# Kernel optimization log

Hardware: AMD Instinct MI355X
Metric: run time of the kernel (lower is better)

## Reference

```python
import jax, jax.numpy as jnp
import numpy as np

N, E = 50000, 1600000
FEAT, HID, HEADS = 256, 64, 2
NEG_SLOPE = 0.2


def gat_conv(x, src, dst, W, att_src, att_dst, bias, heads, out_ch):
    """PyG GATConv (concat=True, self-loops already appended to src/dst)."""
    n = x.shape[0]
    h = (x @ W).reshape(n, heads, out_ch)                      # [N,H,C]
    a_src = jnp.einsum('nhc,hc->nh', h, att_src)               # [N,H]
    a_dst = jnp.einsum('nhc,hc->nh', h, att_dst)               # [N,H]
    alpha = jax.nn.leaky_relu(a_src[src] + a_dst[dst], NEG_SLOPE)  # [E',H]
    # segment softmax over incoming edges of each dst node
    amax = jax.ops.segment_max(alpha, dst, num_segments=n)
    alpha = jnp.exp(alpha - amax[dst])
    denom = jax.ops.segment_sum(alpha, dst, num_segments=n)
    alpha = alpha / (denom[dst] + 1e-16)
    msg = h[src] * alpha[..., None]                            # [E',H,C]
    out = jax.ops.segment_sum(msg, dst, num_segments=n)        # [N,H,C]
    return out.reshape(n, heads * out_ch) + bias


def setup_inputs() -> dict:
    key = jax.random.key(0)
    ks = jax.random.split(key, 10)
    x = jax.random.normal(ks[0], (N, FEAT), dtype=jnp.float32)
    edge_index = jax.random.randint(ks[1], (2, E), 0, N, dtype=jnp.int64)
    s1 = 1.0 / np.sqrt(FEAT)
    s2 = 1.0 / np.sqrt(HID * HEADS)
    sa = 1.0 / np.sqrt(HID)
    return {
        'x': x,
        'edge_index': edge_index,
        'W1': jax.random.uniform(ks[2], (FEAT, HEADS * HID), jnp.float32, -s1, s1),
        'att_src1': jax.random.uniform(ks[3], (HEADS, HID), jnp.float32, -sa, sa),
        'att_dst1': jax.random.uniform(ks[4], (HEADS, HID), jnp.float32, -sa, sa),
        'b1': jnp.zeros((HEADS * HID,), jnp.float32),
        'W2': jax.random.uniform(ks[5], (HEADS * HID, HID), jnp.float32, -s2, s2),
        'att_src2': jax.random.uniform(ks[6], (1, HID), jnp.float32, -sa, sa),
        'att_dst2': jax.random.uniform(ks[7], (1, HID), jnp.float32, -sa, sa),
        'b2': jnp.zeros((HID,), jnp.float32),
    }


def reference(x, edge_index, W1, att_src1, att_dst1, b1, W2, att_src2, att_dst2, b2):
    n = x.shape[0]
    loop = jnp.arange(n, dtype=edge_index.dtype)
    src = jnp.concatenate([edge_index[0], loop])   # add self loops (PyG default)
    dst = jnp.concatenate([edge_index[1], loop])
    h = gat_conv(x, src, dst, W1, att_src1, att_dst1, b1, HEADS, HID)
    h = jax.nn.relu(h)  # dropout is identity in eval mode
    h = gat_conv(h, src, dst, W2, att_src2, att_dst2, b2, 1, HID)
    return jax.nn.log_softmax(h, axis=1)
```

## Files before the change

kernel.cpp:

```cpp
#include <hip/hip_runtime.h>
#include <hip/hip_bf16.h>
#include <math.h>

typedef short bf16x8 __attribute__((ext_vector_type(8)));
typedef float f32x4 __attribute__((ext_vector_type(4)));

#define BSHIFT 7
#define BWIDTH 128
#define PCHUNK 4096

__global__ void prep_kernel(int* __restrict__ bcnt,
                            const float* __restrict__ W1, const float* __restrict__ W2,
                            __hip_bfloat16* __restrict__ W1t,
                            __hip_bfloat16* __restrict__ W2t) {
    if (blockIdx.x == 0) {
        bcnt[threadIdx.x] = 0;
        bcnt[threadIdx.x + 256] = 0;
        return;
    }
    int idx = (blockIdx.x - 1) * 256 + threadIdx.x;
    const int n1 = 128 * 256;
    if (idx < n1) {
        int nn = idx >> 8, kk = idx & 255;
        W1t[idx] = __float2bfloat16(W1[kk * 128 + nn]);
    } else {
        int j = idx - n1;
        if (j < 64 * 128) {
            int nn = j >> 7, kk = j & 127;
            W2t[j] = __float2bfloat16(W2[kk * 64 + nn]);
        }
    }
}

__global__ __launch_bounds__(256) void bucket_hist(const int* __restrict__ ei, int E,
                                                   int* __restrict__ bcnt) {
    __shared__ int h[512];
    int tid = threadIdx.x;
    for (int i = tid; i < 512; i += 256) h[i] = 0;
    __syncthreads();
    int start = blockIdx.x * PCHUNK;
    int cnt = min(PCHUNK, E - start);
    for (int i = tid; i < cnt; i += 256)
        atomicAdd(&h[ei[E + start + i] >> BSHIFT], 1);
    __syncthreads();
    for (int i = tid; i < 512; i += 256)
        if (h[i]) atomicAdd(&bcnt[i], h[i]);
}

__global__ __launch_bounds__(512) void bucket_scan(const int* __restrict__ bcnt,
                                                   int* __restrict__ bbase,
                                                   int* __restrict__ bcur,
                                                   int nbk, int n) {
    __shared__ int s[512];
    int tid = threadIdx.x;
    int nodes = 0;
    if (tid < nbk) nodes = min(BWIDTH, n - (tid << BSHIFT));
    int v = (tid < nbk) ? bcnt[tid] + nodes : 0;
    s[tid] = v;
    __syncthreads();
    #pragma unroll
    for (int o = 1; o < 512; o <<= 1) {
        int t = (tid >= o) ? s[tid - o] : 0;
        __syncthreads();
        s[tid] += t;
        __syncthreads();
    }
    if (tid < nbk) {
        int ex = s[tid] - v;
        bbase[tid] = ex;
        bcur[tid] = ex - (tid << BSHIFT);
    }
    if (tid == nbk) bbase[nbk] = s[tid];
}

__global__ __launch_bounds__(256) void partition_edges(const int* __restrict__ ei, int E,
                                                       int* __restrict__ bcur,
                                                       int* __restrict__ tmp) {
    __shared__ int2 stage[PCHUNK];
    __shared__ int h[512];
    __shared__ int lbase[512];
    int tid = threadIdx.x;
    int start = blockIdx.x * PCHUNK;
    int cnt = min(PCHUNK, E - start);
    for (int i = tid; i < 512; i += 256) h[i] = 0;
    __syncthreads();
    for (int i = tid; i < cnt; i += 256) {
        int s = ei[start + i];
        int d = ei[E + start + i];
        stage[i] = make_int2(s, d);
        atomicAdd(&h[d >> BSHIFT], 1);
    }
    __syncthreads();
    for (int i = tid; i < 512; i += 256) {
        if (h[i] > 0) lbase[i] = atomicAdd(&bcur[i], h[i]);
        h[i] = 0;
    }
    __syncthreads();
    for (int i = tid; i < cnt; i += 256) {
        int2 e = stage[i];
        int b = e.y >> BSHIFT;
        int r = atomicAdd(&h[b], 1);
        tmp[lbase[b] + r] = (e.x << BSHIFT) | (e.y & (BWIDTH - 1));
    }
}

__global__ __launch_bounds__(256) void bucket_csr(const int* __restrict__ bbase,
                                                  const int* __restrict__ tmp,
                                                  int* __restrict__ offs,
                                                  int* __restrict__ srcs,
                                                  int n, int nbk) {
    __shared__ int cnt[BWIDTH];
    __shared__ int sa[BWIDTH];
    __shared__ int cur[BWIDTH];
    int b = blockIdx.x;
    int tid = threadIdx.x;
    int node0 = b << BSHIFT;
    int nnodes = min(BWIDTH, n - node0);
    int cb = bbase[b];
    int ce = bbase[b + 1];
    int tb = cb - node0;
    int ecnt = (ce - cb) - nnodes;

    if (tid < BWIDTH) cnt[tid] = (tid < nnodes) ? 1 : 0;
    __syncthreads();
    for (int i = tid; i < ecnt; i += 256)
        atomicAdd(&cnt[tmp[tb + i] & (BWIDTH - 1)], 1);
    __syncthreads();
    if (tid < BWIDTH) sa[tid] = cnt[tid];
    __syncthreads();
    #pragma unroll
    for (int o = 1; o < BWIDTH; o <<= 1) {
        int v = 0;
        if (tid < BWIDTH) { v = sa[tid]; if (tid >= o) v += sa[tid - o]; }
        __syncthreads();
        if (tid < BWIDTH) sa[tid] = v;
        __syncthreads();
    }
    if (tid < BWIDTH) {
        int ex = sa[tid] - cnt[tid];
        if (tid < nnodes) {
            offs[node0 + tid] = cb + ex;
            srcs[cb + ex] = node0 + tid;
        }
        cur[tid] = ex + (tid < nnodes ? 1 : 0);
    }
    if (b == nbk - 1 && tid == 0) offs[n] = ce;
    __syncthreads();
    for (int i = tid; i < ecnt; i += 256) {
        int e = tmp[tb + i];
        int li = e & (BWIDTH - 1);
        int r = atomicAdd(&cur[li], 1);
        srcs[cb + r] = e >> BSHIFT;
    }
}

template <bool A_BF16, int NT, int HEADS>
__global__ __launch_bounds__(256) void gemm_att(
    const void* __restrict__ Av, const __hip_bfloat16* __restrict__ Bt,
    __hip_bfloat16* __restrict__ C,
    const float* __restrict__ atts, const float* __restrict__ attd,
    float* __restrict__ a_s, float* __restrict__ a_d, int M, int K) {
    constexpr int N = NT * 16;
    __shared__ __hip_bfloat16 As[64][40];
    int tid = threadIdx.x;
    int w = tid >> 6, l = tid & 63;
    int q = l >> 4, m16 = l & 15;
    int bm = blockIdx.x * 64;

    int lr = tid >> 2, lseg = tid & 3;
    int arow = bm + lr; if (arow >= M) arow = M - 1;

    f32x4 acc[NT];
    #pragma unroll
    for (int t = 0; t < NT; t++) acc[t] = (f32x4){0.f, 0.f, 0.f, 0.f};

    for (int kc = 0; kc < K; kc += 32) {
        if (A_BF16) {
            const __hip_bfloat16* A = (const __hip_bfloat16*)Av;
            uint4 v = *(const uint4*)(A + (size_t)arow * K + kc + lseg * 8);
            *(uint4*)&As[lr][lseg * 8] = v;
        } else {
            const float* A = (const float*)Av;
            float4 v0 = *(const float4*)(A + (size_t)arow * K + kc + lseg * 8);
            float4 v1 = *(const float4*)(A + (size_t)arow * K + kc + lseg * 8 + 4);
            union { __hip_bfloat16 h[8]; uint4 u; } tmp;
            tmp.h[0] = __float2bfloat16(v0.x); tmp.h[1] = __float2bfloat16(v0.y);
            tmp.h[2] = __float2bfloat16(v0.z); tmp.h[3] = __float2bfloat16(v0.w);
            tmp.h[4] = __float2bfloat16(v1.x); tmp.h[5] = __float2bfloat16(v1.y);
            tmp.h[6] = __float2bfloat16(v1.z); tmp.h[7] = __float2bfloat16(v1.w);
            *(uint4*)&As[lr][lseg * 8] = tmp.u;
        }
        __syncthreads();
        bf16x8 a = *(const bf16x8*)&As[w * 16 + m16][q * 8];
        #pragma unroll
        for (int t = 0; t < NT; t++) {
            bf16x8 b = *(const bf16x8*)(Bt + (size_t)(t * 16 + m16) * K + kc + q * 8);
            acc[t] = __builtin_amdgcn_mfma_f32_16x16x32_bf16(a, b, acc[t], 0, 0, 0);
        }
        __syncthreads();
    }

    #pragma unroll
    for (int t = 0; t < NT; t++) {
        #pragma unroll
        for (int r = 0; r < 4; r++) {
            int row = bm + w * 16 + q * 4 + r;
            if (row < M) C[(size_t)row * N + t * 16 + m16] = __float2bfloat16(acc[t][r]);
        }
    }

    float ps[HEADS][4], pd[HEADS][4];
    #pragma unroll
    for (int hh = 0; hh < HEADS; hh++)
        #pragma unroll
        for (int r = 0; r < 4; r++) { ps[hh][r] = 0.f; pd[hh][r] = 0.f; }
    #pragma unroll
    for (int t = 0; t < NT; t++) {
        int ch = t * 16 + m16;
        float asw = atts[ch], adw = attd[ch];
        int hh = (HEADS == 2) ? (t >> 2) : 0;
        #pragma unroll
        for (int r = 0; r < 4; r++) {
            ps[hh][r] = fmaf(acc[t][r], asw, ps[hh][r]);
            pd[hh][r] = fmaf(acc[t][r], adw, pd[hh][r]);
        }
    }
    #pragma unroll
    for (int o = 1; o < 16; o <<= 1) {
        #pragma unroll
        for (int hh = 0; hh < HEADS; hh++)
            #pragma unroll
            for (int r = 0; r < 4; r++) {
                ps[hh][r] += __shfl_xor(ps[hh][r], o);
                pd[hh][r] += __shfl_xor(pd[hh][r], o);
            }
    }
    if (m16 == 0) {
        #pragma unroll
        for (int r = 0; r < 4; r++) {
            int row = bm + w * 16 + q * 4 + r;
            if (row < M) {
                if (HEADS == 2) {
                    a_s[row * 2]     = ps[0][r];
                    a_s[row * 2 + 1] = ps[1][r];
                    a_d[row * 2]     = pd[0][r];
                    a_d[row * 2 + 1] = pd[1][r];
                } else {
                    a_s[row] = ps[0][r];
                    a_d[row] = pd[0][r];
                }
            }
        }
    }
}

__device__ __forceinline__ float leaky(float r) {
    return r < 0.f ? 0.2f * r : r;
}

__device__ __forceinline__ void unpack2(unsigned u, float& lo, float& hi) {
    lo = __uint_as_float(u << 16);
    hi = __uint_as_float(u & 0xffff0000u);
}

__global__ __launch_bounds__(256) void edge_agg_l1(
    const int* __restrict__ offs, const int* __restrict__ srcs,
    const __hip_bfloat16* __restrict__ h1, const float* __restrict__ asv,
    const float* __restrict__ adv, const float* __restrict__ bias,
    __hip_bfloat16* __restrict__ out, int n) {
    int d = (blockIdx.x * blockDim.x + threadIdx.x) >> 6;
    int lane = threadIdx.x & 63;
    if (d >= n) return;
    int start = offs[d], end = offs[d + 1];
    float ad0 = adv[2 * d], ad1 = adv[2 * d + 1];

    int sub = lane & 15;
    int g = lane >> 4;
    int ch0 = sub * 8;
    int hsel = sub >> 3;

    float s0 = 0.f, s1 = 0.f;
    float acc[8];
    #pragma unroll
    for (int k = 0; k < 8; k++) acc[k] = 0.f;

    for (int base = start; base < end; base += 64) {
        int cnt = min(64, end - base);
        int s_l = 0;
        float e0 = 0.f, e1 = 0.f;
        if (lane < cnt) {
            s_l = srcs[base + lane];
            float2 a = *(const float2*)(asv + 2 * s_l);
            e0 = __expf(leaky(a.x + ad0));
            e1 = __expf(leaky(a.y + ad1));
        }
        s0 += e0;
        s1 += e1;

        int steps = (cnt + 3) >> 2;
        int jj = 0;
        for (; jj + 2 <= steps; jj += 2) {
            int eA = jj * 4 + g, eB = eA + 4;
            float w0A = __shfl(e0, eA), w1A = __shfl(e1, eA);
            int sA = __shfl(s_l, eA);
            float w0B = __shfl(e0, eB), w1B = __shfl(e1, eB);
            int sB = __shfl(s_l, eB);
            float wA = hsel ? w1A : w0A;
            float wB = hsel ? w1B : w0B;
            uint4 vA = *(const uint4*)(h1 + (size_t)sA * 128 + ch0);
            uint4 vB = *(const uint4*)(h1 + (size_t)sB * 128 + ch0);
            float f0, f1, f2, f3, f4, f5, f6, f7;
            unpack2(vA.x, f0, f1); unpack2(vA.y, f2, f3);
            unpack2(vA.z, f4, f5); unpack2(vA.w, f6, f7);
            acc[0] = fmaf(wA, f0, acc[0]); acc[1] = fmaf(wA, f1, acc[1]);
            acc[2] = fmaf(wA, f2, acc[2]); acc[3] = fmaf(wA, f3, acc[3]);
            acc[4] = fmaf(wA, f4, acc[4]); acc[5] = fmaf(wA, f5, acc[5]);
            acc[6] = fmaf(wA, f6, acc[6]); acc[7] = fmaf(wA, f7, acc[7]);
            unpack2(vB.x, f0, f1); unpack2(vB.y, f2, f3);
            unpack2(vB.z, f4, f5); unpack2(vB.w, f6, f7);
            acc[0] = fmaf(wB, f0, acc[0]); acc[1] = fmaf(wB, f1, acc[1]);
            acc[2] = fmaf(wB, f2, acc[2]); acc[3] = fmaf(wB, f3, acc[3]);
            acc[4] = fmaf(wB, f4, acc[4]); acc[5] = fmaf(wB, f5, acc[5]);
            acc[6] = fmaf(wB, f6, acc[6]); acc[7] = fmaf(wB, f7, acc[7]);
        }
        if (jj < steps) {
            int eA = jj * 4 + g;
            float w0A = __shfl(e0, eA), w1A = __shfl(e1, eA);
            int sA = __shfl(s_l, eA);
            float wA = hsel ? w1A : w0A;
            uint4 vA = *(const uint4*)(h1 + (size_t)sA * 128 + ch0);
            float f0, f1, f2, f3, f4, f5, f6, f7;
            unpack2(vA.x, f0, f1); unpack2(vA.y, f2, f3);
            unpack2(vA.z, f4, f5); unpack2(vA.w, f6, f7);
            acc[0] = fmaf(wA, f0, acc[0]); acc[1] = fmaf(wA, f1, acc[1]);
            acc[2] = fmaf(wA, f2, acc[2]); acc[3] = fmaf(wA, f3, acc[3]);
            acc[4] = fmaf(wA, f4, acc[4]); acc[5] = fmaf(wA, f5, acc[5]);
            acc[6] = fmaf(wA, f6, acc[6]); acc[7] = fmaf(wA, f7, acc[7]);
        }
    }
    #pragma unroll
    for (int o = 16; o < 64; o <<= 1)
        #pragma unroll
        for (int k = 0; k < 8; k++) acc[k] += __shfl_xor(acc[k], o);
    #pragma unroll
    for (int o = 1; o < 64; o <<= 1) {
        s0 += __shfl_xor(s0, o);
        s1 += __shfl_xor(s1, o);
    }

    if (lane < 16) {
        float invh = 1.f / ((hsel ? s1 : s0) + 1e-16f);
        float4 b0 = *(const float4*)(bias + ch0);
        float4 b1 = *(const float4*)(bias + ch0 + 4);
        union { __hip_bfloat16 h[8]; uint4 u; } o2;
        o2.h[0] = __float2bfloat16(fmaxf(fmaf(acc[0], invh, b0.x), 0.f));
        o2.h[1] = __float2bfloat16(fmaxf(fmaf(acc[1], invh, b0.y), 0.f));
        o2.h[2] = __float2bfloat16(fmaxf(fmaf(acc[2], invh, b0.z), 0.f));
        o2.h[3] = __float2bfloat16(fmaxf(fmaf(acc[3], invh, b0.w), 0.f));
        o2.h[4] = __float2bfloat16(fmaxf(fmaf(acc[4], invh, b1.x), 0.f));
        o2.h[5] = __float2bfloat16(fmaxf(fmaf(acc[5], invh, b1.y), 0.f));
        o2.h[6] = __float2bfloat16(fmaxf(fmaf(acc[6], invh, b1.z), 0.f));
        o2.h[7] = __float2bfloat16(fmaxf(fmaf(acc[7], invh, b1.w), 0.f));
        *(uint4*)(out + (size_t)d * 128 + ch0) = o2.u;
    }
}

__global__ __launch_bounds__(256) void edge_agg_l2(
    const int* __restrict__ offs, const int* __restrict__ srcs,
    const __hip_bfloat16* __restrict__ h2, const float* __restrict__ asv,
    const float* __restrict__ adv, const float* __restrict__ bias,
    float* __restrict__ out, int n) {
    int d = (blockIdx.x * blockDim.x + threadIdx.x) >> 6;
    int lane = threadIdx.x & 63;
    if (d >= n) return;
    int start = offs[d], end = offs[d + 1];
    float ad = adv[d];

    int sub = lane & 7;
    int g = lane >> 3;
    int ch0 = sub * 8;

    float ssum = 0.f;
    float acc[8];
    #pragma unroll
    for (int k = 0; k < 8; k++) acc[k] = 0.f;

    for (int base = start; base < end; base += 64) {
        int cnt = min(64, end - base);
        int s_l = 0;
        float ew = 0.f;
        if (lane < cnt) {
            s_l = srcs[base + lane];
            ew = __expf(leaky(asv[s_l] + ad));
        }
        ssum += ew;

        int steps = (cnt + 7) >> 3;
        int jj = 0;
        for (; jj + 2 <= steps; jj += 2) {
            int eA = jj * 8 + g, eB = eA + 8;
            float wA = __shfl(ew, eA);
            int sA = __shfl(s_l, eA);
            float wB = __shfl(ew, eB);
            int sB = __shfl(s_l, eB);
            uint4 vA = *(const uint4*)(h2 + (size_t)sA * 64 + ch0);
            uint4 vB = *(const uint4*)(h2 + (size_t)sB * 64 + ch0);
            float f0, f1, f2, f3, f4, f5, f6, f7;
            unpack2(vA.x, f0, f1); unpack2(vA.y, f2, f3);
            unpack2(vA.z, f4, f5); unpack2(vA.w, f6, f7);
            acc[0] = fmaf(wA, f0, acc[0]); acc[1] = fmaf(wA, f1, acc[1]);
            acc[2] = fmaf(wA, f2, acc[2]); acc[3] = fmaf(wA, f3, acc[3]);
            acc[4] = fmaf(wA, f4, acc[4]); acc[5] = fmaf(wA, f5, acc[5]);
            acc[6] = fmaf(wA, f6, acc[6]); acc[7] = fmaf(wA, f7, acc[7]);
            unpack2(vB.x, f0, f1); unpack2(vB.y, f2, f3);
            unpack2(vB.z, f4, f5); unpack2(vB.w, f6, f7);
            acc[0] = fmaf(wB, f0, acc[0]); acc[1] = fmaf(wB, f1, acc[1]);
            acc[2] = fmaf(wB, f2, acc[2]); acc[3] = fmaf(wB, f3, acc[3]);
            acc[4] = fmaf(wB, f4, acc[4]); acc[5] = fmaf(wB, f5, acc[5]);
            acc[6] = fmaf(wB, f6, acc[6]); acc[7] = fmaf(wB, f7, acc[7]);
        }
        if (jj < steps) {
            int eA = jj * 8 + g;
            float wA = __shfl(ew, eA);
            int sA = __shfl(s_l, eA);
            uint4 vA = *(const uint4*)(h2 + (size_t)sA * 64 + ch0);
            float f0, f1, f2, f3, f4, f5, f6, f7;
            unpack2(vA.x, f0, f1); unpack2(vA.y, f2, f3);
            unpack2(vA.z, f4, f5); unpack2(vA.w, f6, f7);
            acc[0] = fmaf(wA, f0, acc[0]); acc[1] = fmaf(wA, f1, acc[1]);
            acc[2] = fmaf(wA, f2, acc[2]); acc[3] = fmaf(wA, f3, acc[3]);
            acc[4] = fmaf(wA, f4, acc[4]); acc[5] = fmaf(wA, f5, acc[5]);
            acc[6] = fmaf(wA, f6, acc[6]); acc[7] = fmaf(wA, f7, acc[7]);
        }
    }
    #pragma unroll
    for (int o = 8; o < 64; o <<= 1)
        #pragma unroll
        for (int k = 0; k < 8; k++) acc[k] += __shfl_xor(acc[k], o);
    #pragma unroll
    for (int o = 1; o < 64; o <<= 1) ssum += __shfl_xor(ssum, o);

    float inv = 1.f / (ssum + 1e-16f);
    float4 b0 = *(const float4*)(bias + ch0);
    float4 b1 = *(const float4*)(bias + ch0 + 4);
    float v[8];
    v[0] = fmaf(acc[0], inv, b0.x); v[1] = fmaf(acc[1], inv, b0.y);
    v[2] = fmaf(acc[2], inv, b0.z); v[3] = fmaf(acc[3], inv, b0.w);
    v[4] = fmaf(acc[4], inv, b1.x); v[5] = fmaf(acc[5], inv, b1.y);
    v[6] = fmaf(acc[6], inv, b1.z); v[7] = fmaf(acc[7], inv, b1.w);

    float vm = v[0];
    #pragma unroll
    for (int k = 1; k < 8; k++) vm = fmaxf(vm, v[k]);
    #pragma unroll
    for (int o = 1; o < 8; o <<= 1) vm = fmaxf(vm, __shfl_xor(vm, o));
    float se_loc = 0.f;
    #pragma unroll
    for (int k = 0; k < 8; k++) se_loc += __expf(v[k] - vm);
    #pragma unroll
    for (int o = 1; o < 8; o <<= 1) se_loc += __shfl_xor(se_loc, o);
    float lse = vm + logf(se_loc);

    if (lane < 8) {
        float4 o0 = make_float4(v[0] - lse, v[1] - lse, v[2] - lse, v[3] - lse);
        float4 o1 = make_float4(v[4] - lse, v[5] - lse, v[6] - lse, v[7] - lse);
        *(float4*)(out + (size_t)d * 64 + ch0) = o0;
        *(float4*)(out + (size_t)d * 64 + ch0 + 4) = o1;
    }
}

extern "C" void kernel_launch(void* const* d_in, const int* in_sizes, int n_in,
                              void* d_out, int out_size, void* d_ws, size_t ws_size,
                              hipStream_t stream) {
    const float* x    = (const float*)d_in[0];
    const int*   ei   = (const int*)d_in[1];
    const float* W1   = (const float*)d_in[2];
    const float* as1w = (const float*)d_in[3];
    const float* ad1w = (const float*)d_in[4];
    const float* b1   = (const float*)d_in[5];
    const float* W2   = (const float*)d_in[6];
    const float* as2w = (const float*)d_in[7];
    const float* ad2w = (const float*)d_in[8];
    const float* b2   = (const float*)d_in[9];
    float* out = (float*)d_out;

    const int n = in_sizes[0] / 256;
    const int E = in_sizes[1] / 2;
    const int tot = E + n;
    const int nbk = (n + BWIDTH - 1) / BWIDTH;

    char* p = (char*)d_ws;
    auto alloc = [&](size_t bytes) {
        void* r = (void*)p;
        p += (bytes + 255) & ~(size_t)255;
        return r;
    };
    int*   offs  = (int*)alloc((size_t)(n + 1) * 4);
    int*   srcs  = (int*)alloc((size_t)tot * 4);
    int*   tmp   = (int*)alloc((size_t)E * 4);
    int*   bcnt  = (int*)alloc(512 * 4);
    int*   bbase = (int*)alloc(512 * 4);
    int*   bcur  = (int*)alloc(512 * 4);
    __hip_bfloat16* W1t = (__hip_bfloat16*)alloc((size_t)128 * 256 * 2);
    __hip_bfloat16* W2t = (__hip_bfloat16*)alloc((size_t)64 * 128 * 2);
    __hip_bfloat16* h1  = (__hip_bfloat16*)alloc((size_t)n * 128 * 2);
    __hip_bfloat16* out1= (__hip_bfloat16*)alloc((size_t)n * 128 * 2);
    __hip_bfloat16* h2  = (__hip_bfloat16*)alloc((size_t)n * 64 * 2);
    float* a_s1 = (float*)alloc((size_t)n * 2 * 4);
    float* a_d1 = (float*)alloc((size_t)n * 2 * 4);
    float* a_s2 = (float*)alloc((size_t)n * 4);
    float* a_d2 = (float*)alloc((size_t)n * 4);

    int pblocks = (E + PCHUNK - 1) / PCHUNK;

    prep_kernel<<<1 + (128 * 256 + 64 * 128 + 255) / 256, 256, 0, stream>>>(
        bcnt, W1, W2, W1t, W2t);

    bucket_hist<<<pblocks, 256, 0, stream>>>(ei, E, bcnt);
    bucket_scan<<<1, 512, 0, stream>>>(bcnt, bbase, bcur, nbk, n);
    partition_edges<<<pblocks, 256, 0, stream>>>(ei, E, bcur, tmp);
    bucket_csr<<<nbk, 256, 0, stream>>>(bbase, tmp, offs, srcs, n, nbk);

    gemm_att<false, 8, 2><<<(n + 63) / 64, 256, 0, stream>>>(
        x, W1t, h1, as1w, ad1w, a_s1, a_d1, n, 256);
    edge_agg_l1<<<((size_t)n * 64 + 255) / 256, 256, 0, stream>>>(
        offs, srcs, h1, a_s1, a_d1, b1, out1, n);

    gemm_att<true, 4, 1><<<(n + 63) / 64, 256, 0, stream>>>(
        out1, W2t, h2, as2w, ad2w, a_s2, a_d2, n, 128);
    edge_agg_l2<<<((size_t)n * 64 + 255) / 256, 256, 0, stream>>>(
        offs, srcs, h2, a_s2, a_d2, b2, out, n);
}
```

Baseline: 285.6 us.

## Split feature matrices into 32-channel column slabs and aggregate each slab separately

The GEMM now writes h1/h2 in a column-blocked layout of 32-channel slabs, each slab contiguous across nodes. Edge aggregation then runs one launch per slab (four for layer 1, two for layer 2), so each pass gathers from a smaller working set that fits better in cache. The cost is that edge indices and attention exponentials are recomputed in every pass, and there are more kernel launches. The final log-softmax moves into a separate kernel because no single pass sees a full row.

```diff
diff --git a/kernel.cpp b/kernel.cpp
--- a/kernel.cpp
+++ b/kernel.cpp
@@ -160,7 +160,6 @@
     __hip_bfloat16* __restrict__ C,
     const float* __restrict__ atts, const float* __restrict__ attd,
     float* __restrict__ a_s, float* __restrict__ a_d, int M, int K) {
-    constexpr int N = NT * 16;
     __shared__ __hip_bfloat16 As[64][40];
     int tid = threadIdx.x;
     int w = tid >> 6, l = tid & 63;
@@ -177,7 +176,8 @@
     for (int kc = 0; kc < K; kc += 32) {
         if (A_BF16) {
             const __hip_bfloat16* A = (const __hip_bfloat16*)Av;
-            uint4 v = *(const uint4*)(A + (size_t)arow * K + kc + lseg * 8);
+            uint4 v = *(const uint4*)(A + (size_t)(kc >> 5) * M * 32 +
+                                      (size_t)arow * 32 + lseg * 8);
             *(uint4*)&As[lr][lseg * 8] = v;
         } else {
             const float* A = (const float*)Av;
@@ -202,10 +202,12 @@
 
     #pragma unroll
     for (int t = 0; t < NT; t++) {
+        int ch = t * 16 + m16;
+        size_t cbase = (size_t)(ch >> 5) * M * 32 + (ch & 31);
         #pragma unroll
         for (int r = 0; r < 4; r++) {
             int row = bm + w * 16 + q * 4 + r;
-            if (row < M) C[(size_t)row * N + t * 16 + m16] = __float2bfloat16(acc[t][r]);
+            if (row < M) C[cbase + (size_t)row * 32] = __float2bfloat16(acc[t][r]);
         }
     }
 
@@ -263,21 +265,20 @@
     hi = __uint_as_float(u & 0xffff0000u);
 }
 
-__global__ __launch_bounds__(256) void edge_agg_l1(
+__global__ __launch_bounds__(256) void edge_agg_l1_c(
     const int* __restrict__ offs, const int* __restrict__ srcs,
-    const __hip_bfloat16* __restrict__ h1, const float* __restrict__ asv,
-    const float* __restrict__ adv, const float* __restrict__ bias,
-    __hip_bfloat16* __restrict__ out, int n) {
+    const __hip_bfloat16* __restrict__ hc, const float* __restrict__ asv,
+    const float* __restrict__ adv, const float* __restrict__ biasc,
+    __hip_bfloat16* __restrict__ outc, int n, int hsel) {
     int d = (blockIdx.x * blockDim.x + threadIdx.x) >> 6;
     int lane = threadIdx.x & 63;
     if (d >= n) return;
     int start = offs[d], end = offs[d + 1];
     float ad0 = adv[2 * d], ad1 = adv[2 * d + 1];
 
-    int sub = lane & 15;
-    int g = lane >> 4;
+    int sub = lane & 3;
+    int g = lane >> 2;
     int ch0 = sub * 8;
-    int hsel = sub >> 3;
 
     float s0 = 0.f, s1 = 0.f;
     float acc[8];
@@ -296,19 +297,18 @@
         }
         s0 += e0;
         s1 += e1;
-
-        int steps = (cnt + 3) >> 2;
+        float esel = hsel ? e1 : e0;
+
+        int steps = (cnt + 15) >> 4;
         int jj = 0;
         for (; jj + 2 <= steps; jj += 2) {
-            int eA = jj * 4 + g, eB = eA + 4;
-            float w0A = __shfl(e0, eA), w1A = __shfl(e1, eA);
+            int eA = jj * 16 + g, eB = eA + 16;
+            float wA = __shfl(esel, eA);
             int sA = __shfl(s_l, eA);
-            float w0B = __shfl(e0, eB), w1B = __shfl(e1, eB);
+            float wB = __shfl(esel, eB);
             int sB = __shfl(s_l, eB);
-            float wA = hsel ? w1A : w0A;
-            float wB = hsel ? w1B : w0B;
-            uint4 vA = *(const uint4*)(h1 + (size_t)sA * 128 + ch0);
-            uint4 vB = *(const uint4*)(h1 + (size_t)sB * 128 + ch0);
+            uint4 vA = *(const uint4*)(hc + (size_t)sA * 32 + ch0);
+            uint4 vB = *(const uint4*)(hc + (size_t)sB * 32 + ch0);
             float f0, f1, f2, f3, f4, f5, f6, f7;
             unpack2(vA.x, f0, f1); unpack2(vA.y, f2, f3);
             unpack2(vA.z, f4, f5); unpack2(vA.w, f6, f7);
@@ -324,11 +324,10 @@
             acc[6] = fmaf(wB, f6, acc[6]); acc[7] = fmaf(wB, f7, acc[7]);
         }
         if (jj < steps) {
-            int eA = jj * 4 + g;
-            float w0A = __shfl(e0, eA), w1A = __shfl(e1, eA);
+            int eA = jj * 16 + g;
+            float wA = __shfl(esel, eA);
             int sA = __shfl(s_l, eA);
-            float wA = hsel ? w1A : w0A;
-            uint4 vA = *(const uint4*)(h1 + (size_t)sA * 128 + ch0);
+            uint4 vA = *(const uint4*)(hc + (size_t)sA * 32 + ch0);
             float f0, f1, f2, f3, f4, f5, f6, f7;
             unpack2(vA.x, f0, f1); unpack2(vA.y, f2, f3);
             unpack2(vA.z, f4, f5); unpack2(vA.w, f6, f7);
@@ -339,7 +338,7 @@
         }
     }
     #pragma unroll
-    for (int o = 16; o < 64; o <<= 1)
+    for (int o = 4; o < 64; o <<= 1)
         #pragma unroll
         for (int k = 0; k < 8; k++) acc[k] += __shfl_xor(acc[k], o);
     #pragma unroll
@@ -348,36 +347,36 @@
         s1 += __shfl_xor(s1, o);
     }
 
-    if (lane < 16) {
-        float invh = 1.f / ((hsel ? s1 : s0) + 1e-16f);
-        float4 b0 = *(const float4*)(bias + ch0);
-        float4 b1 = *(const float4*)(bias + ch0 + 4);
+    if (lane < 4) {
+        float inv = 1.f / ((hsel ? s1 : s0) + 1e-16f);
+        float4 b0 = *(const float4*)(biasc + ch0);
+        float4 b1 = *(const float4*)(biasc + ch0 + 4);
         union { __hip_bfloat16 h[8]; uint4 u; } o2;
-        o2.h[0] = __float2bfloat16(fmaxf(fmaf(acc[0], invh, b0.x), 0.f));
-        o2.h[1] = __float2bfloat16(fmaxf(fmaf(acc[1], invh, b0.y), 0.f));
-        o2.h[2] = __float2bfloat16(fmaxf(fmaf(acc[2], invh, b0.z), 0.f));
-        o2.h[3] = __float2bfloat16(fmaxf(fmaf(acc[3], invh, b0.w), 0.f));
-        o2.h[4] = __float2bfloat16(fmaxf(fmaf(acc[4], invh, b1.x), 0.f));
-        o2.h[5] = __float2bfloat16(fmaxf(fmaf(acc[5], invh, b1.y), 0.f));
-        o2.h[6] = __float2bfloat16(fmaxf(fmaf(acc[6], invh, b1.z), 0.f));
-        o2.h[7] = __float2bfloat16(fmaxf(fmaf(acc[7], invh, b1.w), 0.f));
-        *(uint4*)(out + (size_t)d * 128 + ch0) = o2.u;
-    }
-}
-
-__global__ __launch_bounds__(256) void edge_agg_l2(
+        o2.h[0] = __float2bfloat16(fmaxf(fmaf(acc[0], inv, b0.x), 0.f));
+        o2.h[1] = __float2bfloat16(fmaxf(fmaf(acc[1], inv, b0.y), 0.f));
+        o2.h[2] = __float2bfloat16(fmaxf(fmaf(acc[2], inv, b0.z), 0.f));
+        o2.h[3] = __float2bfloat16(fmaxf(fmaf(acc[3], inv, b0.w), 0.f));
+        o2.h[4] = __float2bfloat16(fmaxf(fmaf(acc[4], inv, b1.x), 0.f));
+        o2.h[5] = __float2bfloat16(fmaxf(fmaf(acc[5], inv, b1.y), 0.f));
+        o2.h[6] = __float2bfloat16(fmaxf(fmaf(acc[6], inv, b1.z), 0.f));
+        o2.h[7] = __float2bfloat16(fmaxf(fmaf(acc[7], inv, b1.w), 0.f));
+        *(uint4*)(outc + (size_t)d * 32 + ch0) = o2.u;
+    }
+}
+
+__global__ __launch_bounds__(256) void edge_agg_l2_c(
     const int* __restrict__ offs, const int* __restrict__ srcs,
-    const __hip_bfloat16* __restrict__ h2, const float* __restrict__ asv,
-    const float* __restrict__ adv, const float* __restrict__ bias,
-    float* __restrict__ out, int n) {
+    const __hip_bfloat16* __restrict__ hc, const float* __restrict__ asv,
+    const float* __restrict__ adv, const float* __restrict__ biasc,
+    float* __restrict__ outc, int n) {
     int d = (blockIdx.x * blockDim.x + threadIdx.x) >> 6;
     int lane = threadIdx.x & 63;
     if (d >= n) return;
     int start = offs[d], end = offs[d + 1];
     float ad = adv[d];
 
-    int sub = lane & 7;
-    int g = lane >> 3;
+    int sub = lane & 3;
+    int g = lane >> 2;
     int ch0 = sub * 8;
 
     float ssum = 0.f;
@@ -395,16 +394,16 @@
         }
         ssum += ew;
 
-        int steps = (cnt + 7) >> 3;
+        int steps = (cnt + 15) >> 4;
         int jj = 0;
         for (; jj + 2 <= steps; jj += 2) {
-            int eA = jj * 8 + g, eB = eA + 8;
+            int eA = jj * 16 + g, eB = eA + 16;
             float wA = __shfl(ew, eA);
             int sA = __shfl(s_l, eA);
             float wB = __shfl(ew, eB);
             int sB = __shfl(s_l, eB);
-            uint4 vA = *(const uint4*)(h2 + (size_t)sA * 64 + ch0);
-            uint4 vB = *(const uint4*)(h2 + (size_t)sB * 64 + ch0);
+            uint4 vA = *(const uint4*)(hc + (size_t)sA * 32 + ch0);
+            uint4 vB = *(const uint4*)(hc + (size_t)sB * 32 + ch0);
             float f0, f1, f2, f3, f4, f5, f6, f7;
             unpack2(vA.x, f0, f1); unpack2(vA.y, f2, f3);
             unpack2(vA.z, f4, f5); unpack2(vA.w, f6, f7);
@@ -420,10 +419,10 @@
             acc[6] = fmaf(wB, f6, acc[6]); acc[7] = fmaf(wB, f7, acc[7]);
         }
         if (jj < steps) {
-            int eA = jj * 8 + g;
+            int eA = jj * 16 + g;
             float wA = __shfl(ew, eA);
             int sA = __shfl(s_l, eA);
-            uint4 vA = *(const uint4*)(h2 + (size_t)sA * 64 + ch0);
+            uint4 vA = *(const uint4*)(hc + (size_t)sA * 32 + ch0);
             float f0, f1, f2, f3, f4, f5, f6, f7;
             unpack2(vA.x, f0, f1); unpack2(vA.y, f2, f3);
             unpack2(vA.z, f4, f5); unpack2(vA.w, f6, f7);
@@ -434,39 +433,50 @@
         }
     }
     #pragma unroll
-    for (int o = 8; o < 64; o <<= 1)
+    for (int o = 4; o < 64; o <<= 1)
         #pragma unroll
         for (int k = 0; k < 8; k++) acc[k] += __shfl_xor(acc[k], o);
     #pragma unroll
     for (int o = 1; o < 64; o <<= 1) ssum += __shfl_xor(ssum, o);
 
-    float inv = 1.f / (ssum + 1e-16f);
-    float4 b0 = *(const float4*)(bias + ch0);
-    float4 b1 = *(const float4*)(bias + ch0 + 4);
-    float v[8];
-    v[0] = fmaf(acc[0], inv, b0.x); v[1] = fmaf(acc[1], inv, b0.y);
-    v[2] = fmaf(acc[2], inv, b0.z); v[3] = fmaf(acc[3], inv, b0.w);
-    v[4] = fmaf(acc[4], inv, b1.x); v[5] = fmaf(acc[5], inv, b1.y);
-    v[6] = fmaf(acc[6], inv, b1.z); v[7] = fmaf(acc[7], inv, b1.w);
-
-    float vm = v[0];
-    #pragma unroll
-    for (int k = 1; k < 8; k++) vm = fmaxf(vm, v[k]);
-    #pragma unroll
-    for (int o = 1; o < 8; o <<= 1) vm = fmaxf(vm, __shfl_xor(vm, o));
-    float se_loc = 0.f;
-    #pragma unroll
-    for (int k = 0; k < 8; k++) se_loc += __expf(v[k] - vm);
-    #pragma unroll
-    for (int o = 1; o < 8; o <<= 1) se_loc += __shfl_xor(se_loc, o);
-    float lse = vm + logf(se_loc);
-
-    if (lane < 8) {
-        float4 o0 = make_float4(v[0] - lse, v[1] - lse, v[2] - lse, v[3] - lse);
-        float4 o1 = make_float4(v[4] - lse, v[5] - lse, v[6] - lse, v[7] - lse);
-        *(float4*)(out + (size_t)d * 64 + ch0) = o0;
-        *(float4*)(out + (size_t)d * 64 + ch0 + 4) = o1;
-    }
+    if (lane < 4) {
+        float inv = 1.f / (ssum + 1e-16f);
+        float4 b0 = *(const float4*)(biasc + ch0);
+        float4 b1 = *(const float4*)(biasc + ch0 + 4);
+        float* o = outc + (size_t)d * 64 + ch0;
+        float4 o0 = make_float4(fmaf(acc[0], inv, b0.x), fmaf(acc[1], inv, b0.y),
+                                fmaf(acc[2], inv, b0.z), fmaf(acc[3], inv, b0.w));
+        float4 o1 = make_float4(fmaf(acc[4], inv, b1.x), fmaf(acc[5], inv, b1.y),
+                                fmaf(acc[6], inv, b1.z), fmaf(acc[7], inv, b1.w));
+        *(float4*)o = o0;
+        *(float4*)(o + 4) = o1;
+    }
+}
+
+__global__ __launch_bounds__(256) void log_softmax_k(float* __restrict__ out, int n) {
+    int idx = blockIdx.x * blockDim.x + threadIdx.x;
+    int d = idx >> 3;
+    int sl = idx & 7;
+    if (d >= n) return;
+    float* p = out + (size_t)d * 64 + sl * 8;
+    float4 a = *(const float4*)p;
+    float4 b = *(const float4*)(p + 4);
+    float v[8] = {a.x, a.y, a.z, a.w, b.x, b.y, b.z, b.w};
+    float m = v[0];
+    #pragma unroll
+    for (int k = 1; k < 8; k++) m = fmaxf(m, v[k]);
+    #pragma unroll
+    for (int o = 1; o < 8; o <<= 1) m = fmaxf(m, __shfl_xor(m, o));
+    float s = 0.f;
+    #pragma unroll
+    for (int k = 0; k < 8; k++) s += __expf(v[k] - m);
+    #pragma unroll
+    for (int o = 1; o < 8; o <<= 1) s += __shfl_xor(s, o);
+    float lse = m + logf(s);
+    float4 o0 = make_float4(v[0] - lse, v[1] - lse, v[2] - lse, v[3] - lse);
+    float4 o1 = make_float4(v[4] - lse, v[5] - lse, v[6] - lse, v[7] - lse);
+    *(float4*)p = o0;
+    *(float4*)(p + 4) = o1;
 }
 
 extern "C" void kernel_launch(void* const* d_in, const int* in_sizes, int n_in,
@@ -512,6 +522,7 @@
     float* a_d2 = (float*)alloc((size_t)n * 4);
 
     int pblocks = (E + PCHUNK - 1) / PCHUNK;
+    int agg_blocks = (int)(((size_t)n * 64 + 255) / 256);
 
     prep_kernel<<<1 + (128 * 256 + 64 * 128 + 255) / 256, 256, 0, stream>>>(
         bcnt, W1, W2, W1t, W2t);
@@ -523,11 +534,18 @@
 
     gemm_att<false, 8, 2><<<(n + 63) / 64, 256, 0, stream>>>(
         x, W1t, h1, as1w, ad1w, a_s1, a_d1, n, 256);
-    edge_agg_l1<<<((size_t)n * 64 + 255) / 256, 256, 0, stream>>>(
-        offs, srcs, h1, a_s1, a_d1, b1, out1, n);
+    for (int c = 0; c < 4; c++) {
+        edge_agg_l1_c<<<agg_blocks, 256, 0, stream>>>(
+            offs, srcs, h1 + (size_t)c * n * 32, a_s1, a_d1, b1 + c * 32,
+            out1 + (size_t)c * n * 32, n, c >> 1);
+    }
 
     gemm_att<true, 4, 1><<<(n + 63) / 64, 256, 0, stream>>>(
         out1, W2t, h2, as2w, ad2w, a_s2, a_d2, n, 128);
-    edge_agg_l2<<<((size_t)n * 64 + 255) / 256, 256, 0, stream>>>(
-        offs, srcs, h2, a_s2, a_d2, b2, out, n);
-}
+    for (int c = 0; c < 2; c++) {
+        edge_agg_l2_c<<<agg_blocks, 256, 0, stream>>>(
+            offs, srcs, h2 + (size_t)c * n * 32, a_s2, a_d2, b2 + c * 32,
+            out + c * 32, n);
+    }
+    log_softmax_k<<<(int)(((size_t)n * 8 + 255) / 256), 256, 0, stream>>>(out, n);
+}
```

New measurement: 382.4 us. 1.34x slower.
